# Performance work log

Hardware: AMD Instinct MI355X
Metric: run time of the kernel (lower is better)

The kernel has to match this reference:

```python
import jax, jax.numpy as jnp
import numpy as np

N_NODES = 20000
N_EDGES = 320000
N_INPUT = 128
N_HIDDEN = 128
N_LAYERS = 3
N_OUT = 2
C_WEIGHT = 1.0
BN_EPS = 1e-5


def _psi(z):
    # sign(z) * log(1 + |z|), the LorentzNet scalar map
    return jnp.sign(z) * jnp.log1p(jnp.abs(z))


def _mink_dot(a, b):
    # Minkowski inner product, metric diag(+1, -1, ..., -1)
    return a[:, 0] * b[:, 0] - jnp.sum(a[:, 1:] * b[:, 1:], axis=1)


def setup_inputs() -> dict:
    key = jax.random.key(0)
    ks = jax.random.split(key, 12)
    n, h, L = N_INPUT, N_HIDDEN, N_LAYERS
    d_in = 2 * n + 6
    f32 = jnp.float32
    inp = {
        "x": jax.random.normal(ks[0], (N_NODES, n), f32),
        "edge_index": jax.random.randint(ks[1], (2, N_EDGES), 0, N_NODES),
        "edge_attr": jax.random.normal(ks[2], (N_EDGES, 4), f32),
        # phi_e: Linear(d_in->h, no bias), BN(h), ReLU, Linear(h->h), ReLU
        "W1": (jax.random.normal(ks[3], (L, d_in, h), f32) / np.sqrt(d_in)).astype(f32),
        "gamma": jnp.ones((L, h), f32),
        "beta": jnp.zeros((L, h), f32),
        "W2": (jax.random.normal(ks[4], (L, h, h), f32) / np.sqrt(h)).astype(f32),
        "b2": jnp.zeros((L, h), f32),
        # phi_x: Linear(h->h), ReLU, Linear(h->1, no bias, xavier gain 1e-3)
        "Wa": (jax.random.normal(ks[5], (L, h, h), f32) / np.sqrt(h)).astype(f32),
        "ba": jnp.zeros((L, h), f32),
        "Wb": (jax.random.normal(ks[6], (L, h, 1), f32) * 1e-3).astype(f32),
        # phi_m: Linear(h->1), Sigmoid
        "Wm": (jax.random.normal(ks[7], (L, h, 1), f32) / np.sqrt(h)).astype(f32),
        "bm": jnp.zeros((L, 1), f32),
        # final edge_mlp: Linear(h -> N_OUT)
        "We": (jax.random.normal(ks[8], (h, N_OUT), f32) / np.sqrt(h)).astype(f32),
        "be": jnp.zeros((N_OUT,), f32),
    }
    return inp


def _lgeb_layer(x, row, col, edge_attr, W1, gamma, beta, W2, b2, Wa, ba, Wb, Wm, bm):
    x_i = x[row]                       # [E, n] gather (aggregation target)
    x_j = x[col]                       # [E, n]
    x_diff = x_i - x_j                 # [E, n]
    norms = _psi(_mink_dot(x_diff, x_diff))[:, None]   # [E, 1]
    dots = _psi(_mink_dot(x_i, x_j))[:, None]          # [E, 1]
    m = jnp.concatenate([x_i, x_j, edge_attr, norms, dots], axis=1)  # [E, 2n+6]
    # phi_e
    hpre = m @ W1                                       # [E, h]
    mu = jnp.mean(hpre, axis=0)
    var = jnp.mean(jnp.square(hpre - mu), axis=0)       # biased, torch BN train mode
    hbn = (hpre - mu) * jax.lax.rsqrt(var + BN_EPS) * gamma + beta
    hid = jax.nn.relu(hbn)
    m_ij = jax.nn.relu(hid @ W2 + b2)                   # [E, h]
    # phi_m gate
    w = jax.nn.sigmoid(m_ij @ Wm + bm)                  # [E, 1]
    m_ij = m_ij * w
    # phi_x scalar weight on x_diff
    s = jax.nn.relu(m_ij @ Wa + ba) @ Wb                # [E, 1]
    trans = jnp.clip(x_diff * s, -100.0, 100.0)         # [E, n]
    x_agg = jax.ops.segment_sum(trans, row, num_segments=x.shape[0])  # [N, n]
    return x + C_WEIGHT * x_agg


def reference(x, edge_index, edge_attr, W1, gamma, beta, W2, b2,
              Wa, ba, Wb, Wm, bm, We, be):
    row, col = edge_index[0], edge_index[1]
    for l in range(N_LAYERS):
        x = _lgeb_layer(x, row, col, edge_attr,
                        W1[l], gamma[l], beta[l], W2[l], b2[l],
                        Wa[l], ba[l], Wb[l], Wm[l], bm[l])
    return jax.nn.sigmoid(x @ We + be)                  # [N, N_OUT]


if __name__ == "__main__":
    out = reference(**setup_inputs())
    print(out.shape, out.dtype)
```

## Files before the change

kernel.cpp:

```cpp
#include <hip/hip_runtime.h>
#include <math.h>

#define NND 20000
#define NE  320000
#define NF  128
#define EPS 1e-5f
#define TE  64
#define NT  256
#define NTILES (NE / TE)
#define NGRP (NE / 4)
#define XST 136
#define BST 40

typedef short short8 __attribute__((ext_vector_type(8)));
typedef float float4v __attribute__((ext_vector_type(4)));

__device__ __forceinline__ float psif(float z) {
    return copysignf(log1pf(fabsf(z)), z);
}
__device__ __forceinline__ float sigm(float z) {
    return 1.f / (1.f + expf(-z));
}
__device__ __forceinline__ short f2bf(float f) {
    union { float f; unsigned u; } v; v.f = f;
    unsigned r = v.u + 0x7fffu + ((v.u >> 16) & 1u);
    return (short)(r >> 16);
}
__device__ __forceinline__ float bf2f(short u) {
    union { unsigned u; float f; } v; v.u = ((unsigned)(unsigned short)u) << 16;
    return v.f;
}
__device__ __forceinline__ float clipf(float v) {
    return fminf(fmaxf(v, -100.f), 100.f);
}

__device__ __forceinline__ void stage_b(const unsigned short* __restrict__ wsrc, int wstride,
                                        int ks, short* bt, int t) {
    #pragma unroll
    for (int rr = 0; rr < 2; ++rr) {
        int c = t + rr * 256;
        int n = c >> 2, h = c & 3;
        short8 v = *(const short8*)(wsrc + (size_t)n * wstride + ks * 32 + h * 8);
        *(short8*)(bt + n * BST + h * 8) = v;
    }
}

__device__ __forceinline__ void ldreg_b(const unsigned short* __restrict__ w, int wstride,
                                        int ks, int t, short8* r) {
    #pragma unroll
    for (int rr = 0; rr < 2; ++rr) {
        int c = t + rr * 256;
        int n = c >> 2, h = c & 3;
        r[rr] = *(const short8*)(w + (size_t)n * wstride + ks * 32 + h * 8);
    }
}
__device__ __forceinline__ void wrlds_b(short* bt, int t, const short8* r) {
    #pragma unroll
    for (int rr = 0; rr < 2; ++rr) {
        int c = t + rr * 256;
        int n = c >> 2, h = c & 3;
        *(short8*)(bt + n * BST + h * 8) = r[rr];
    }
}

__global__ __launch_bounds__(NT, 2)
void node_gemm(const float* __restrict__ x,
               const unsigned short* __restrict__ wt,
               float* __restrict__ P,
               unsigned short* __restrict__ rec,
               float* __restrict__ gstats)
{
    __shared__ short lxa[TE * XST];
    __shared__ short lbt[128 * BST];

    const int t = threadIdx.x;
    const int lane = t & 63, quad = lane >> 4, ln15 = lane & 15;
    const int wv = t >> 6, we = wv >> 1, wc = wv & 1;
    const int n0 = blockIdx.x * 64;
    const int ch = blockIdx.y;
    const unsigned short* wsrc = wt + (size_t)ch * 128 * 128;

    if (blockIdx.x == 0 && ch == 0) gstats[t] = 0.f;

    {
        int row = t >> 2, q = t & 3;
        int src = min(n0 + row, NND - 1);
        const float4* xp = (const float4*)(x + (size_t)src * NF) + q * 8;
        #pragma unroll
        for (int u = 0; u < 4; ++u) {
            float4 a = xp[2*u], b = xp[2*u+1];
            short8 s;
            s[0]=f2bf(a.x); s[1]=f2bf(a.y); s[2]=f2bf(a.z); s[3]=f2bf(a.w);
            s[4]=f2bf(b.x); s[5]=f2bf(b.y); s[6]=f2bf(b.z); s[7]=f2bf(b.w);
            *(short8*)(lxa + row * XST + q * 32 + u * 8) = s;
        }
    }

    float4v acc[2][4];
    #pragma unroll
    for (int a = 0; a < 2; ++a)
        #pragma unroll
        for (int b = 0; b < 4; ++b) { float4v z = {0.f,0.f,0.f,0.f}; acc[a][b] = z; }

    for (int ks = 0; ks < 4; ++ks) {
        __syncthreads();
        stage_b(wsrc, NF, ks, lbt, t);
        __syncthreads();
        short8 af[2], bfr[4];
        #pragma unroll
        for (int ef = 0; ef < 2; ++ef)
            af[ef] = *(const short8*)(lxa + (we*32 + ef*16 + ln15) * XST + ks*32 + quad*8);
        #pragma unroll
        for (int fc = 0; fc < 4; ++fc)
            bfr[fc] = *(const short8*)(lbt + (wc*64 + fc*16 + ln15) * BST + quad*8);
        #pragma unroll
        for (int ef = 0; ef < 2; ++ef)
            #pragma unroll
            for (int fc = 0; fc < 4; ++fc)
                acc[ef][fc] = __builtin_amdgcn_mfma_f32_16x16x32_bf16(af[ef], bfr[fc], acc[ef][fc], 0, 0, 0);
    }
    #pragma unroll
    for (int fc = 0; fc < 4; ++fc) {
        int c = wc * 64 + fc * 16 + ln15;
        #pragma unroll
        for (int ef = 0; ef < 2; ++ef)
            #pragma unroll
            for (int rg = 0; rg < 4; ++rg) {
                int nrow = n0 + we * 32 + ef * 16 + quad * 4 + rg;
                if (nrow < NND) {
                    if (ch == 0)
                        P[(size_t)nrow * NF + c] = acc[ef][fc][rg];
                    else
                        rec[(size_t)nrow * 256 + 128 + c] =
                            (unsigned short)f2bf(acc[ef][fc][rg]);
                }
            }
    }
}

__global__ __launch_bounds__(NT)
void pack_x(const float* __restrict__ x, unsigned short* __restrict__ rec)
{
    int i = blockIdx.x * NT + threadIdx.x;
    if (i >= NND * 16) return;
    int n = i >> 4, q = i & 15;
    const float4* xp = (const float4*)(x + (size_t)n * NF + q * 8);
    float4 a = xp[0], b = xp[1];
    short8 s;
    s[0]=f2bf(a.x); s[1]=f2bf(a.y); s[2]=f2bf(a.z); s[3]=f2bf(a.w);
    s[4]=f2bf(b.x); s[5]=f2bf(b.y); s[6]=f2bf(b.z); s[7]=f2bf(b.w);
    *(short8*)(rec + (size_t)n * 256 + q * 8) = s;
}

__global__ __launch_bounds__(NT, 4)
void edge_pass(const float* __restrict__ x,
               const float* __restrict__ P,
               const unsigned short* __restrict__ rec,
               const int* __restrict__ rowS,
               const int* __restrict__ colS,
               const float* __restrict__ eaS,
               const float* __restrict__ W1l,
               unsigned short* __restrict__ hpre,
               float* __restrict__ gstats)
{
    __shared__ float sred[4][256];

    const int t = threadIdx.x;
    const int lane = t & 63;
    const int wv = t >> 6;
    const int gg = lane >> 4;
    const int ln15 = lane & 15;
    const int c0 = ln15 * 8;

    float w6[6][8];
    #pragma unroll
    for (int k = 0; k < 6; ++k) {
        const float4* wp = (const float4*)(W1l + (size_t)(256 + k) * NF + c0);
        float4 a = wp[0], b = wp[1];
        w6[k][0] = a.x; w6[k][1] = a.y; w6[k][2] = a.z; w6[k][3] = a.w;
        w6[k][4] = b.x; w6[k][5] = b.y; w6[k][6] = b.z; w6[k][7] = b.w;
    }

    float ss[8], sq[8];
    #pragma unroll
    for (int i = 0; i < 8; ++i) { ss[i] = 0.f; sq[i] = 0.f; }

    const int wid = blockIdx.x * 4 + wv;
    const int nw  = gridDim.x * 4;

    for (int g = wid; g < NGRP; g += nw) {
        const int e = g * 4 + gg;
        const int r = rowS[e];
        const int c = colS[e];
        const float4* xip = (const float4*)(x + (size_t)r * NF + c0);
        const float4* prp = (const float4*)(P + (size_t)r * NF + c0);
        short8 xjb = *(const short8*)(rec + (size_t)c * 256 + c0);
        short8 qjb = *(const short8*)(rec + (size_t)c * 256 + 128 + c0);
        float4 xi0 = xip[0], xi1 = xip[1];
        float4 pr0 = prp[0], pr1 = prp[1];
        float4 ea  = ((const float4*)eaS)[e];

        float xiv[8] = {xi0.x, xi0.y, xi0.z, xi0.w, xi1.x, xi1.y, xi1.z, xi1.w};
        float xjv[8];
        #pragma unroll
        for (int i = 0; i < 8; ++i) xjv[i] = bf2f(xjb[i]);

        float nrm = 0.f, dot = 0.f;
        #pragma unroll
        for (int i = 0; i < 8; ++i) {
            float d = xiv[i] - xjv[i];
            nrm = fmaf(-d, d, nrm);
            dot = fmaf(-xiv[i], xjv[i], dot);
        }
        if (ln15 == 0) {
            float d0 = xiv[0] - xjv[0];
            nrm += 2.f * d0 * d0;
            dot += 2.f * xiv[0] * xjv[0];
        }
        nrm += __shfl_xor(nrm, 1); nrm += __shfl_xor(nrm, 2);
        nrm += __shfl_xor(nrm, 4); nrm += __shfl_xor(nrm, 8);
        dot += __shfl_xor(dot, 1); dot += __shfl_xor(dot, 2);
        dot += __shfl_xor(dot, 4); dot += __shfl_xor(dot, 8);
        const float pn = psif(nrm), pd = psif(dot);

        float prv[8] = {pr0.x, pr0.y, pr0.z, pr0.w, pr1.x, pr1.y, pr1.z, pr1.w};

        short8 o;
        #pragma unroll
        for (int i = 0; i < 8; ++i) {
            float v = prv[i] + bf2f(qjb[i]);
            v = fmaf(ea.x, w6[0][i], v);
            v = fmaf(ea.y, w6[1][i], v);
            v = fmaf(ea.z, w6[2][i], v);
            v = fmaf(ea.w, w6[3][i], v);
            v = fmaf(pn,   w6[4][i], v);
            v = fmaf(pd,   w6[5][i], v);
            ss[i] += v;
            sq[i] = fmaf(v, v, sq[i]);
            o[i] = f2bf(v);
        }
        *(short8*)(hpre + (size_t)e * NF + c0) = o;
    }

    #pragma unroll
    for (int i = 0; i < 8; ++i) {
        ss[i] += __shfl_xor(ss[i], 16); ss[i] += __shfl_xor(ss[i], 32);
        sq[i] += __shfl_xor(sq[i], 16); sq[i] += __shfl_xor(sq[i], 32);
    }
    if (lane < 16) {
        #pragma unroll
        for (int i = 0; i < 8; ++i) {
            sred[wv][c0 + i]       = ss[i];
            sred[wv][128 + c0 + i] = sq[i];
        }
    }
    __syncthreads();
    atomicAdd(&gstats[t], sred[0][t] + sred[1][t] + sred[2][t] + sred[3][t]);
}

__global__ __launch_bounds__(NT, 4)
void passB(const unsigned short* __restrict__ hpre,
           const float* __restrict__ gstats,
           const float* __restrict__ gamma,
           const float* __restrict__ beta,
           const unsigned short* __restrict__ wt2,
           const float* __restrict__ b2,
           const unsigned short* __restrict__ wta,
           const float* __restrict__ ba,
           const float* __restrict__ wb,
           const float* __restrict__ wm,
           const float* __restrict__ bm,
           float* __restrict__ sG)
{
    __shared__ short lxi[TE * XST];
    __shared__ short lbt0[128 * BST];
    __shared__ short lbt1[128 * BST];
    __shared__ float gpart[2][TE];
    __shared__ float spart[2][TE];
    __shared__ float wgt[TE];
    __shared__ float scs[NF], sfs[NF];

    const int t = threadIdx.x;
    const int lane = t & 63, quad = lane >> 4, ln15 = lane & 15;
    const int wv = t >> 6, we = wv >> 1, wc = wv & 1;
    const int e0 = blockIdx.x * TE;
    const float bmv = bm[0];

    if (t < NF) {
        float mu  = gstats[t] * (1.f / NE);
        float var = fmaxf(gstats[128 + t] * (1.f / NE) - mu * mu, 0.f);
        float inv = rsqrtf(var + EPS);
        float sc  = gamma[t] * inv;
        scs[t] = sc;
        sfs[t] = beta[t] - mu * sc;
    }
    __syncthreads();

    {
        const int le = t >> 2, q = t & 3;
        const unsigned short* hp = hpre + (size_t)(e0 + le) * NF + q * 32;
        #pragma unroll
        for (int h = 0; h < 4; ++h) {
            short8 v = *(const short8*)(hp + h * 8);
            short o[8];
            #pragma unroll
            for (int i = 0; i < 8; ++i) {
                int chn = q * 32 + h * 8 + i;
                float f = fmaxf(fmaf(bf2f(v[i]), scs[chn], sfs[chn]), 0.f);
                o[i] = f2bf(f);
            }
            *(short8*)(lxi + le * XST + q * 32 + h * 8) = *(short8*)o;
        }
    }

    float4v acc[2][4];
    #pragma unroll
    for (int a = 0; a < 2; ++a)
        #pragma unroll
        for (int b = 0; b < 4; ++b) { float4v z = {0.f,0.f,0.f,0.f}; acc[a][b] = z; }

    {
        short8 pre[2];
        ldreg_b(wt2, NF, 0, t, pre);
        wrlds_b(lbt0, t, pre);
        __syncthreads();
        for (int ks = 0; ks < 4; ++ks) {
            short8 nxt[2];
            if (ks < 3) ldreg_b(wt2, NF, ks + 1, t, nxt);
            const short* cur = (ks & 1) ? lbt1 : lbt0;
            short8 af[2], bfr[4];
            #pragma unroll
            for (int ef = 0; ef < 2; ++ef)
                af[ef] = *(const short8*)(lxi + (we*32 + ef*16 + ln15) * XST + ks*32 + quad*8);
            #pragma unroll
            for (int fc = 0; fc < 4; ++fc)
                bfr[fc] = *(const short8*)(cur + (wc*64 + fc*16 + ln15) * BST + quad*8);
            #pragma unroll
            for (int ef = 0; ef < 2; ++ef)
                #pragma unroll
                for (int fc = 0; fc < 4; ++fc)
                    acc[ef][fc] = __builtin_amdgcn_mfma_f32_16x16x32_bf16(af[ef], bfr[fc], acc[ef][fc], 0, 0, 0);
            if (ks < 3) wrlds_b((ks & 1) ? lbt0 : lbt1, t, nxt);
            __syncthreads();
        }
    }

    {
        float p[2][4] = {{0.f,0.f,0.f,0.f},{0.f,0.f,0.f,0.f}};
        #pragma unroll
        for (int fc = 0; fc < 4; ++fc) {
            int c = wc * 64 + fc * 16 + ln15;
            float bb = b2[c], wmv = wm[c];
            #pragma unroll
            for (int ef = 0; ef < 2; ++ef)
                #pragma unroll
                for (int rg = 0; rg < 4; ++rg) {
                    int r = we * 32 + ef * 16 + quad * 4 + rg;
                    float v = fmaxf(acc[ef][fc][rg] + bb, 0.f);
                    lxi[r * XST + c] = f2bf(v);
                    p[ef][rg] = fmaf(v, wmv, p[ef][rg]);
                }
        }
        #pragma unroll
        for (int ef = 0; ef < 2; ++ef)
            #pragma unroll
            for (int rg = 0; rg < 4; ++rg) {
                p[ef][rg] += __shfl_xor(p[ef][rg], 1);
                p[ef][rg] += __shfl_xor(p[ef][rg], 2);
                p[ef][rg] += __shfl_xor(p[ef][rg], 4);
                p[ef][rg] += __shfl_xor(p[ef][rg], 8);
            }
        if (ln15 == 0) {
            #pragma unroll
            for (int ef = 0; ef < 2; ++ef)
                #pragma unroll
                for (int rg = 0; rg < 4; ++rg)
                    gpart[wc][we * 32 + ef * 16 + quad * 4 + rg] = p[ef][rg];
        }
    }

    #pragma unroll
    for (int a = 0; a < 2; ++a)
        #pragma unroll
        for (int b = 0; b < 4; ++b) { float4v z = {0.f,0.f,0.f,0.f}; acc[a][b] = z; }
    {
        short8 pre[2];
        ldreg_b(wta, NF, 0, t, pre);
        wrlds_b(lbt0, t, pre);
        __syncthreads();
        if (t < TE) wgt[t] = sigm(gpart[0][t] + gpart[1][t] + bmv);
        for (int ks = 0; ks < 4; ++ks) {
            short8 nxt[2];
            if (ks < 3) ldreg_b(wta, NF, ks + 1, t, nxt);
            const short* cur = (ks & 1) ? lbt1 : lbt0;
            short8 af[2], bfr[4];
            #pragma unroll
            for (int ef = 0; ef < 2; ++ef)
                af[ef] = *(const short8*)(lxi + (we*32 + ef*16 + ln15) * XST + ks*32 + quad*8);
            #pragma unroll
            for (int fc = 0; fc < 4; ++fc)
                bfr[fc] = *(const short8*)(cur + (wc*64 + fc*16 + ln15) * BST + quad*8);
            #pragma unroll
            for (int ef = 0; ef < 2; ++ef)
                #pragma unroll
                for (int fc = 0; fc < 4; ++fc)
                    acc[ef][fc] = __builtin_amdgcn_mfma_f32_16x16x32_bf16(af[ef], bfr[fc], acc[ef][fc], 0, 0, 0);
            if (ks < 3) wrlds_b((ks & 1) ? lbt0 : lbt1, t, nxt);
            __syncthreads();
        }
    }
    {
        float p[2][4] = {{0.f,0.f,0.f,0.f},{0.f,0.f,0.f,0.f}};
        #pragma unroll
        for (int fc = 0; fc < 4; ++fc) {
            int c = wc * 64 + fc * 16 + ln15;
            float bav = ba[c], wbv = wb[c];
            #pragma unroll
            for (int ef = 0; ef < 2; ++ef)
                #pragma unroll
                for (int rg = 0; rg < 4; ++rg) {
                    int r = we * 32 + ef * 16 + quad * 4 + rg;
                    float v = fmaxf(fmaf(wgt[r], acc[ef][fc][rg], bav), 0.f);
                    p[ef][rg] = fmaf(v, wbv, p[ef][rg]);
                }
        }
        #pragma unroll
        for (int ef = 0; ef < 2; ++ef)
            #pragma unroll
            for (int rg = 0; rg < 4; ++rg) {
                p[ef][rg] += __shfl_xor(p[ef][rg], 1);
                p[ef][rg] += __shfl_xor(p[ef][rg], 2);
                p[ef][rg] += __shfl_xor(p[ef][rg], 4);
                p[ef][rg] += __shfl_xor(p[ef][rg], 8);
            }
        if (ln15 == 0) {
            #pragma unroll
            for (int ef = 0; ef < 2; ++ef)
                #pragma unroll
                for (int rg = 0; rg < 4; ++rg)
                    spart[wc][we * 32 + ef * 16 + quad * 4 + rg] = p[ef][rg];
        }
    }
    __syncthreads();
    if (t < TE) sG[e0 + t] = spart[0][t] + spart[1][t];
}

__global__ __launch_bounds__(NT)
void hist_k(const int* __restrict__ ei, int* __restrict__ deg)
{
    int e = blockIdx.x * NT + threadIdx.x;
    if (e < NE) atomicAdd(&deg[ei[e]], 1);
}

__global__ __launch_bounds__(NT)
void scan_k(const int* __restrict__ deg, int* __restrict__ rowstart,
            int* __restrict__ cursor)
{
    __shared__ int part[NT];
    const int t = threadIdx.x;
    const int CH = (NND + NT - 1) / NT;
    const int base = t * CH;
    int sum = 0;
    for (int i = 0; i < CH; ++i) {
        int idx = base + i;
        if (idx < NND) sum += deg[idx];
    }
    part[t] = sum;
    __syncthreads();
    int pre = 0;
    for (int j = 0; j < t; ++j) pre += part[j];
    int run = pre;
    for (int i = 0; i < CH; ++i) {
        int idx = base + i;
        if (idx < NND) {
            rowstart[idx] = run;
            cursor[idx]   = run;
            run += deg[idx];
        }
    }
    if (t == NT - 1) rowstart[NND] = run;
}

__global__ __launch_bounds__(NT)
void fill_k(const int* __restrict__ ei, int* __restrict__ cursor,
            int* __restrict__ perm)
{
    int e = blockIdx.x * NT + threadIdx.x;
    if (e < NE) {
        int pos = atomicAdd(&cursor[ei[e]], 1);
        perm[pos] = e;
    }
}

__global__ __launch_bounds__(NT)
void prep_edges(const int* __restrict__ ei, const float* __restrict__ eattr,
                const int* __restrict__ perm,
                int* __restrict__ rowS, int* __restrict__ colS,
                float* __restrict__ eaS)
{
    int p = blockIdx.x * NT + threadIdx.x;
    if (p >= NE) return;
    int e = perm[p];
    rowS[p] = ei[e];
    colS[p] = ei[NE + e];
    ((float4*)eaS)[p] = ((const float4*)eattr)[e];
}

__global__ __launch_bounds__(NT)
void aggregate_k(const float* __restrict__ x,
                 const float* __restrict__ sG,
                 const int* __restrict__ rowstart,
                 const int* __restrict__ colS,
                 float* __restrict__ xn,
                 unsigned short* __restrict__ rec)
{
    const int w  = (blockIdx.x * NT + threadIdx.x) >> 6;
    const int ln = threadIdx.x & 63;
    if (w >= NND) return;
    const int beg = rowstart[w], end = rowstart[w + 1];
    const float* xr = x + (size_t)w * NF;
    const float xr0 = xr[ln], xr1 = xr[ln + 64];
    float a0 = 0.f, a1 = 0.f;
    int p = beg;
    if (p < end) {
        int c = colS[p];
        float v0 = x[(size_t)c * NF + ln];
        float v1 = x[(size_t)c * NF + 64 + ln];
        for (; p + 1 < end; ++p) {
            int c2 = colS[p + 1];
            float w0 = x[(size_t)c2 * NF + ln];
            float w1 = x[(size_t)c2 * NF + 64 + ln];
            float s = sG[p];
            a0 += clipf((xr0 - v0) * s);
            a1 += clipf((xr1 - v1) * s);
            v0 = w0; v1 = w1;
        }
        float s = sG[p];
        a0 += clipf((xr0 - v0) * s);
        a1 += clipf((xr1 - v1) * s);
    }
    const float o0 = xr0 + a0;
    const float o1 = xr1 + a1;
    xn[(size_t)w * NF + ln]      = o0;
    xn[(size_t)w * NF + ln + 64] = o1;
    rec[(size_t)w * 256 + ln]      = (unsigned short)f2bf(o0);
    rec[(size_t)w * 256 + 64 + ln] = (unsigned short)f2bf(o1);
}

__global__ __launch_bounds__(NT)
void aggregate_final(const float* __restrict__ x,
                     const float* __restrict__ sG,
                     const int* __restrict__ rowstart,
                     const int* __restrict__ colS,
                     const float* __restrict__ We,
                     const float* __restrict__ be,
                     float* __restrict__ out)
{
    const int w  = (blockIdx.x * NT + threadIdx.x) >> 6;
    const int ln = threadIdx.x & 63;
    if (w >= NND) return;
    const int beg = rowstart[w], end = rowstart[w + 1];
    const float* xr = x + (size_t)w * NF;
    const float xr0 = xr[ln], xr1 = xr[ln + 64];
    float a0 = 0.f, a1 = 0.f;
    int p = beg;
    if (p < end) {
        int c = colS[p];
        float v0 = x[(size_t)c * NF + ln];
        float v1 = x[(size_t)c * NF + 64 + ln];
        for (; p + 1 < end; ++p) {
            int c2 = colS[p + 1];
            float w0 = x[(size_t)c2 * NF + ln];
            float w1 = x[(size_t)c2 * NF + 64 + ln];
            float s = sG[p];
            a0 += clipf((xr0 - v0) * s);
            a1 += clipf((xr1 - v1) * s);
            v0 = w0; v1 = w1;
        }
        float s = sG[p];
        a0 += clipf((xr0 - v0) * s);
        a1 += clipf((xr1 - v1) * s);
    }
    const float v0 = xr0 + a0;
    const float v1 = xr1 + a1;
    float o0 = v0 * We[ln * 2]     + v1 * We[(ln + 64) * 2];
    float o1 = v0 * We[ln * 2 + 1] + v1 * We[(ln + 64) * 2 + 1];
    #pragma unroll
    for (int m = 1; m < 64; m <<= 1) { o0 += __shfl_xor(o0, m); o1 += __shfl_xor(o1, m); }
    if (ln == 0) {
        out[w * 2]     = sigm(o0 + be[0]);
        out[w * 2 + 1] = sigm(o1 + be[1]);
    }
}

__global__ __launch_bounds__(NT)
void prep_w1n(const float* __restrict__ W1, unsigned short* __restrict__ wt)
{
    int i = blockIdx.x * NT + threadIdx.x;
    if (i >= 3 * 256 * 128) return;
    int l = i / (256 * 128);
    int r = i % (256 * 128);
    int cc = r / 128, k = r % 128;
    int srow = (cc < 128) ? k : 128 + k;
    int scol = (cc < 128) ? cc : cc - 128;
    wt[i] = (unsigned short)f2bf(W1[((size_t)l * 262 + srow) * 128 + scol]);
}

__global__ __launch_bounds__(NT)
void prep_w128(const float* __restrict__ W, unsigned short* __restrict__ wt)
{
    int i = blockIdx.x * NT + threadIdx.x;
    if (i >= 3 * 128 * 128) return;
    int l = i / (128 * 128);
    int r = i % (128 * 128);
    int n = r / 128, k = r % 128;
    wt[i] = (unsigned short)f2bf(W[((size_t)l * 128 + k) * 128 + n]);
}

extern "C" void kernel_launch(void* const* d_in, const int* in_sizes, int n_in,
                              void* d_out, int out_size, void* d_ws, size_t ws_size,
                              hipStream_t stream) {
    const float* x   = (const float*)d_in[0];
    const int*   ei  = (const int*)d_in[1];
    const float* ea  = (const float*)d_in[2];
    const float* W1  = (const float*)d_in[3];
    const float* ga  = (const float*)d_in[4];
    const float* bet = (const float*)d_in[5];
    const float* W2  = (const float*)d_in[6];
    const float* b2  = (const float*)d_in[7];
    const float* Wa  = (const float*)d_in[8];
    const float* ba  = (const float*)d_in[9];
    const float* Wb  = (const float*)d_in[10];
    const float* Wm  = (const float*)d_in[11];
    const float* bm  = (const float*)d_in[12];
    const float* We  = (const float*)d_in[13];
    const float* be  = (const float*)d_in[14];
    float* out = (float*)d_out;

    char* base = (char*)d_ws;
    size_t off = 0;
    auto alloc = [&](size_t bytes) -> void* {
        off = (off + 31) & ~(size_t)31;
        void* p = base + off;
        off += bytes;
        return p;
    };
    float* gstats   = (float*)alloc(256 * sizeof(float));
    int*   deg      = (int*)alloc(NND * sizeof(int));
    int*   rowstart = (int*)alloc((NND + 1) * sizeof(int));
    int*   cursor   = (int*)alloc(NND * sizeof(int));
    int*   perm     = (int*)alloc(NE * sizeof(int));
    int*   rowS     = (int*)alloc(NE * sizeof(int));
    int*   colS     = (int*)alloc(NE * sizeof(int));
    float* eaS      = (float*)alloc((size_t)NE * 4 * sizeof(float));
    float* sG       = (float*)alloc(NE * sizeof(float));
    float* xA       = (float*)alloc((size_t)NND * NF * sizeof(float));
    float* xB       = (float*)alloc((size_t)NND * NF * sizeof(float));
    float* P        = (float*)alloc((size_t)NND * NF * sizeof(float));
    unsigned short* rec  = (unsigned short*)alloc((size_t)NND * 256 * 2);
    unsigned short* wt1n = (unsigned short*)alloc((size_t)3 * 256 * 128 * 2);
    unsigned short* wt2  = (unsigned short*)alloc((size_t)3 * 128 * 128 * 2);
    unsigned short* wta  = (unsigned short*)alloc((size_t)3 * 128 * 128 * 2);
    unsigned short* hpreG= (unsigned short*)alloc((size_t)NE * NF * 2);

    prep_w1n <<<(3 * 256 * 128 + NT - 1) / NT, NT, 0, stream>>>(W1, wt1n);
    prep_w128<<<(3 * 128 * 128 + NT - 1) / NT, NT, 0, stream>>>(W2, wt2);
    prep_w128<<<(3 * 128 * 128 + NT - 1) / NT, NT, 0, stream>>>(Wa, wta);

    hipMemsetAsync(deg, 0, NND * sizeof(int), stream);
    hist_k<<<(NE + NT - 1) / NT, NT, 0, stream>>>(ei, deg);
    scan_k<<<1, NT, 0, stream>>>(deg, rowstart, cursor);
    fill_k<<<(NE + NT - 1) / NT, NT, 0, stream>>>(ei, cursor, perm);
    prep_edges<<<(NE + NT - 1) / NT, NT, 0, stream>>>(ei, ea, perm, rowS, colS, eaS);
    pack_x<<<(NND * 16 + NT - 1) / NT, NT, 0, stream>>>(x, rec);

    const float* xc = x;
    float* buf[2] = { xA, xB };

    for (int l = 0; l < 3; ++l) {
        node_gemm<<<dim3((NND + 63) / 64, 2), NT, 0, stream>>>(
            xc, wt1n + (size_t)l * 256 * 128, P, rec, gstats);
        edge_pass<<<2048, NT, 0, stream>>>(xc, P, rec, rowS, colS, eaS,
                                           W1 + (size_t)l * 262 * 128, hpreG, gstats);
        passB<<<NTILES, NT, 0, stream>>>(hpreG, gstats, ga + l * NF, bet + l * NF,
                                         wt2 + (size_t)l * 128 * 128, b2 + l * NF,
                                         wta + (size_t)l * 128 * 128, ba + l * NF,
                                         Wb + l * NF, Wm + l * NF, bm + l, sG);
        if (l < 2) {
            float* xn = buf[l & 1];
            aggregate_k<<<(NND * 64 + NT - 1) / NT, NT, 0, stream>>>(xc, sG, rowstart,
                                                                     colS, xn, rec);
            xc = xn;
        } else {
            aggregate_final<<<(NND * 64 + NT - 1) / NT, NT, 0, stream>>>(xc, sG, rowstart,
                                                                         colS, We, be, out);
        }
    }
}
```

Before: 749.2 us.

## Software-pipeline edge_pass gathers with double-buffered edge loads and packed row/col indices

Restructures the edge_pass loop so each wave keeps two edges in flight. It issues the gathers for the next edge and prefetches its row/col indices before computing the current one, to hide gather latency. Row and column indices are packed into a single int2 array so one load fetches both. The grid is cut from 2048 to 768 blocks and the occupancy hint from 4 to 3 blocks per CU, giving more registers per thread for the doubled live state at the cost of fewer resident waves.

```diff
diff --git a/kernel.cpp b/kernel.cpp
--- a/kernel.cpp
+++ b/kernel.cpp
@@ -9,6 +9,7 @@
 #define NT  256
 #define NTILES (NE / TE)
 #define NGRP (NE / 4)
+#define EGRID 768
 #define XST 136
 #define BST 40
 
@@ -152,12 +153,74 @@
     *(short8*)(rec + (size_t)n * 256 + q * 8) = s;
 }
 
-__global__ __launch_bounds__(NT, 4)
+struct ED { float4 xi0, xi1, pr0, pr1, ea; short8 xj, qj; };
+
+__device__ __forceinline__ void issue_edge(const float* __restrict__ x,
+                                           const float* __restrict__ P,
+                                           const unsigned short* __restrict__ rec,
+                                           const float* __restrict__ eaS,
+                                           int e, int2 rc, int c0, ED& d)
+{
+    const float4* xip = (const float4*)(x + (size_t)rc.x * NF + c0);
+    const float4* prp = (const float4*)(P + (size_t)rc.x * NF + c0);
+    const short8* rj  = (const short8*)(rec + (size_t)rc.y * 256 + c0);
+    d.xi0 = xip[0]; d.xi1 = xip[1];
+    d.pr0 = prp[0]; d.pr1 = prp[1];
+    d.xj  = rj[0];  d.qj  = rj[16];
+    d.ea  = ((const float4*)eaS)[e];
+}
+
+__device__ __forceinline__ void compute_edge(const ED& d, int e, int ln15, int c0,
+                                             const float (&w6)[6][8],
+                                             float (&ss)[8], float (&sq)[8],
+                                             unsigned short* __restrict__ hpre)
+{
+    float xiv[8] = {d.xi0.x, d.xi0.y, d.xi0.z, d.xi0.w,
+                    d.xi1.x, d.xi1.y, d.xi1.z, d.xi1.w};
+    float nrm = 0.f, dot = 0.f;
+    #pragma unroll
+    for (int i = 0; i < 8; ++i) {
+        float xj = bf2f(d.xj[i]);
+        float dd = xiv[i] - xj;
+        nrm = fmaf(-dd, dd, nrm);
+        dot = fmaf(-xiv[i], xj, dot);
+    }
+    if (ln15 == 0) {
+        float xj0 = bf2f(d.xj[0]);
+        float d0 = xiv[0] - xj0;
+        nrm += 2.f * d0 * d0;
+        dot += 2.f * xiv[0] * xj0;
+    }
+    nrm += __shfl_xor(nrm, 1); nrm += __shfl_xor(nrm, 2);
+    nrm += __shfl_xor(nrm, 4); nrm += __shfl_xor(nrm, 8);
+    dot += __shfl_xor(dot, 1); dot += __shfl_xor(dot, 2);
+    dot += __shfl_xor(dot, 4); dot += __shfl_xor(dot, 8);
+    const float pn = psif(nrm), pd = psif(dot);
+
+    float prv[8] = {d.pr0.x, d.pr0.y, d.pr0.z, d.pr0.w,
+                    d.pr1.x, d.pr1.y, d.pr1.z, d.pr1.w};
+    short8 o;
+    #pragma unroll
+    for (int i = 0; i < 8; ++i) {
+        float v = prv[i] + bf2f(d.qj[i]);
+        v = fmaf(d.ea.x, w6[0][i], v);
+        v = fmaf(d.ea.y, w6[1][i], v);
+        v = fmaf(d.ea.z, w6[2][i], v);
+        v = fmaf(d.ea.w, w6[3][i], v);
+        v = fmaf(pn,     w6[4][i], v);
+        v = fmaf(pd,     w6[5][i], v);
+        ss[i] += v;
+        sq[i] = fmaf(v, v, sq[i]);
+        o[i] = f2bf(v);
+    }
+    *(short8*)(hpre + (size_t)e * NF + c0) = o;
+}
+
+__global__ __launch_bounds__(NT, 3)
 void edge_pass(const float* __restrict__ x,
                const float* __restrict__ P,
                const unsigned short* __restrict__ rec,
-               const int* __restrict__ rowS,
-               const int* __restrict__ colS,
+               const int2* __restrict__ rcS,
                const float* __restrict__ eaS,
                const float* __restrict__ W1l,
                unsigned short* __restrict__ hpre,
@@ -187,59 +250,34 @@
 
     const int wid = blockIdx.x * 4 + wv;
     const int nw  = gridDim.x * 4;
-
-    for (int g = wid; g < NGRP; g += nw) {
-        const int e = g * 4 + gg;
-        const int r = rowS[e];
-        const int c = colS[e];
-        const float4* xip = (const float4*)(x + (size_t)r * NF + c0);
-        const float4* prp = (const float4*)(P + (size_t)r * NF + c0);
-        short8 xjb = *(const short8*)(rec + (size_t)c * 256 + c0);
-        short8 qjb = *(const short8*)(rec + (size_t)c * 256 + 128 + c0);
-        float4 xi0 = xip[0], xi1 = xip[1];
-        float4 pr0 = prp[0], pr1 = prp[1];
-        float4 ea  = ((const float4*)eaS)[e];
-
-        float xiv[8] = {xi0.x, xi0.y, xi0.z, xi0.w, xi1.x, xi1.y, xi1.z, xi1.w};
-        float xjv[8];
-        #pragma unroll
-        for (int i = 0; i < 8; ++i) xjv[i] = bf2f(xjb[i]);
-
-        float nrm = 0.f, dot = 0.f;
-        #pragma unroll
-        for (int i = 0; i < 8; ++i) {
-            float d = xiv[i] - xjv[i];
-            nrm = fmaf(-d, d, nrm);
-            dot = fmaf(-xiv[i], xjv[i], dot);
-        }
-        if (ln15 == 0) {
-            float d0 = xiv[0] - xjv[0];
-            nrm += 2.f * d0 * d0;
-            dot += 2.f * xiv[0] * xjv[0];
-        }
-        nrm += __shfl_xor(nrm, 1); nrm += __shfl_xor(nrm, 2);
-        nrm += __shfl_xor(nrm, 4); nrm += __shfl_xor(nrm, 8);
-        dot += __shfl_xor(dot, 1); dot += __shfl_xor(dot, 2);
-        dot += __shfl_xor(dot, 4); dot += __shfl_xor(dot, 8);
-        const float pn = psif(nrm), pd = psif(dot);
-
-        float prv[8] = {pr0.x, pr0.y, pr0.z, pr0.w, pr1.x, pr1.y, pr1.z, pr1.w};
-
-        short8 o;
-        #pragma unroll
-        for (int i = 0; i < 8; ++i) {
-            float v = prv[i] + bf2f(qjb[i]);
-            v = fmaf(ea.x, w6[0][i], v);
-            v = fmaf(ea.y, w6[1][i], v);
-            v = fmaf(ea.z, w6[2][i], v);
-            v = fmaf(ea.w, w6[3][i], v);
-            v = fmaf(pn,   w6[4][i], v);
-            v = fmaf(pd,   w6[5][i], v);
-            ss[i] += v;
-            sq[i] = fmaf(v, v, sq[i]);
-            o[i] = f2bf(v);
-        }
-        *(short8*)(hpre + (size_t)e * NF + c0) = o;
+    const int s2  = 2 * nw;
+
+    ED A, B;
+    int2 rcA = {0, 0}, rcB = {0, 0}, rcA2 = {0, 0}, rcB2 = {0, 0};
+    int gA = wid, gB = wid + nw;
+
+    if (gA < NGRP) {
+        rcA = rcS[gA * 4 + gg];
+        issue_edge(x, P, rec, eaS, gA * 4 + gg, rcA, c0, A);
+    }
+    if (gB < NGRP) rcB = rcS[gB * 4 + gg];
+
+    while (gA < NGRP) {
+        if (gB < NGRP)
+            issue_edge(x, P, rec, eaS, gB * 4 + gg, rcB, c0, B);
+        int gA2 = gA + s2;
+        if (gA2 < NGRP) rcA2 = rcS[gA2 * 4 + gg];
+        compute_edge(A, gA * 4 + gg, ln15, c0, w6, ss, sq, hpre);
+        gA = gA2;
+        if (gA < NGRP) {
+            rcA = rcA2;
+            issue_edge(x, P, rec, eaS, gA * 4 + gg, rcA, c0, A);
+        }
+        int gB2 = gB + s2;
+        if (gB2 < NGRP) rcB2 = rcS[gB2 * 4 + gg];
+        if (gB < NGRP)
+            compute_edge(B, gB * 4 + gg, ln15, c0, w6, ss, sq, hpre);
+        gB = gB2; rcB = rcB2;
     }
 
     #pragma unroll
@@ -495,14 +533,16 @@
 __global__ __launch_bounds__(NT)
 void prep_edges(const int* __restrict__ ei, const float* __restrict__ eattr,
                 const int* __restrict__ perm,
-                int* __restrict__ rowS, int* __restrict__ colS,
+                int2* __restrict__ rcS, int* __restrict__ colS,
                 float* __restrict__ eaS)
 {
     int p = blockIdx.x * NT + threadIdx.x;
     if (p >= NE) return;
     int e = perm[p];
-    rowS[p] = ei[e];
-    colS[p] = ei[NE + e];
+    int r = ei[e];
+    int c = ei[NE + e];
+    rcS[p] = make_int2(r, c);
+    colS[p] = c;
     ((float4*)eaS)[p] = ((const float4*)eattr)[e];
 }
 
@@ -650,7 +690,7 @@
     int*   rowstart = (int*)alloc((NND + 1) * sizeof(int));
     int*   cursor   = (int*)alloc(NND * sizeof(int));
     int*   perm     = (int*)alloc(NE * sizeof(int));
-    int*   rowS     = (int*)alloc(NE * sizeof(int));
+    int2*  rcS      = (int2*)alloc((size_t)NE * sizeof(int2));
     int*   colS     = (int*)alloc(NE * sizeof(int));
     float* eaS      = (float*)alloc((size_t)NE * 4 * sizeof(float));
     float* sG       = (float*)alloc(NE * sizeof(float));
@@ -671,7 +711,7 @@
     hist_k<<<(NE + NT - 1) / NT, NT, 0, stream>>>(ei, deg);
     scan_k<<<1, NT, 0, stream>>>(deg, rowstart, cursor);
     fill_k<<<(NE + NT - 1) / NT, NT, 0, stream>>>(ei, cursor, perm);
-    prep_edges<<<(NE + NT - 1) / NT, NT, 0, stream>>>(ei, ea, perm, rowS, colS, eaS);
+    prep_edges<<<(NE + NT - 1) / NT, NT, 0, stream>>>(ei, ea, perm, rcS, colS, eaS);
     pack_x<<<(NND * 16 + NT - 1) / NT, NT, 0, stream>>>(x, rec);
 
     const float* xc = x;
@@ -680,8 +720,8 @@
     for (int l = 0; l < 3; ++l) {
         node_gemm<<<dim3((NND + 63) / 64, 2), NT, 0, stream>>>(
             xc, wt1n + (size_t)l * 256 * 128, P, rec, gstats);
-        edge_pass<<<2048, NT, 0, stream>>>(xc, P, rec, rowS, colS, eaS,
-                                           W1 + (size_t)l * 262 * 128, hpreG, gstats);
+        edge_pass<<<EGRID, NT, 0, stream>>>(xc, P, rec, rcS, eaS,
+                                            W1 + (size_t)l * 262 * 128, hpreG, gstats);
         passB<<<NTILES, NT, 0, stream>>>(hpreG, gstats, ga + l * NF, bet + l * NF,
                                          wt2 + (size_t)l * 128 * 128, b2 + l * NF,
                                          wta + (size_t)l * 128 * 128, ba + l * NF,
```

Result: faster. 722.5 us (-3.6%).
